# Kernel optimization log

Hardware: AMD Instinct MI355X
Metric: run time of the kernel (lower is better)

## Reference

```python
import jax, jax.numpy as jnp
import numpy as np

B, S, H, A = 64, 2048, 512, 512


def setup_inputs() -> dict:
    key = jax.random.key(0)
    k1, k2, k3, k4, k5 = jax.random.split(key, 5)
    nn_outs = jax.random.normal(k1, (B, S, H), dtype=jnp.float32)
    # lengths in [1, S] so every row has at least one valid step
    batch_lens = jax.random.randint(k2, (B,), 1, S + 1, dtype=jnp.int64)
    # learned params: context vector ~ U(-0.1, 0.1), Linear(H -> A)
    context = jax.random.uniform(k3, (A,), dtype=jnp.float32, minval=-0.1, maxval=0.1)
    proj_w = jax.random.uniform(k4, (A, H), dtype=jnp.float32, minval=-0.1, maxval=0.1)
    proj_b = jax.random.uniform(k5, (A,), dtype=jnp.float32, minval=-0.1, maxval=0.1)
    return {"nn_outs": nn_outs, "batch_lens": batch_lens,
            "context": context, "proj_w": proj_w, "proj_b": proj_b}


def reference(nn_outs, batch_lens, context, proj_w, proj_b):
    # proj = tanh(Linear(nn_outs)): (B, S, A)
    proj = jnp.tanh(jnp.einsum('bsh,ah->bsa', nn_outs, proj_w) + proj_b)
    # attention scores: (B, S)
    scores = jnp.einsum('bsa,a->bs', proj, context)
    # variable-length masked softmax (replaces the per-batch python loop)
    mask = jnp.arange(nn_outs.shape[1])[None, :] < batch_lens[:, None]  # (B, S)
    scores = jnp.where(mask, scores, -jnp.inf)
    atten = jax.nn.softmax(scores, axis=-1)
    atten = jnp.where(mask, atten, 0.0)  # padded positions exactly zero
    # weighted sum over steps: (B, H)
    return jnp.einsum('bs,bsh->bh', atten, nn_outs)
```

## Files before the change

kernel.cpp:

```cpp
#include <hip/hip_runtime.h>

#define BB 64
#define SS 2048
#define HH 512
#define MROWS (BB*SS)

typedef __attribute__((ext_vector_type(8))) short short8;
typedef __attribute__((ext_vector_type(4))) float f32x4;

__device__ inline unsigned short f2bf(float f){
  unsigned int u = __float_as_uint(f);
  u += 0x7FFFu + ((u >> 16) & 1u);
  return (unsigned short)(u >> 16);
}

__device__ inline int read_len(const void* lens, int i){
  const int* p = (const int*)lens;
  if (p[1] == 0) return (int)((const long long*)lens)[i];
  return p[i];
}

__device__ inline float fast_tanh(float x){
  x = fminf(fmaxf(x, -15.f), 15.f);
  float e = __expf(2.f * x);
  return (e - 1.f) / (e + 1.f);
}

__device__ inline void gload16(const void* gptr, void* lptr){
  __builtin_amdgcn_global_load_lds(
      (const __attribute__((address_space(1))) void*)gptr,
      (__attribute__((address_space(3))) void*)lptr, 16, 0, 0);
}

__device__ inline short8 cvt8p(float4 x0, float4 x1){
  short8 r;
  r[0] = (short)f2bf(x0.x); r[1] = (short)f2bf(x0.y);
  r[2] = (short)f2bf(x0.z); r[3] = (short)f2bf(x0.w);
  r[4] = (short)f2bf(x1.x); r[5] = (short)f2bf(x1.y);
  r[6] = (short)f2bf(x1.z); r[7] = (short)f2bf(x1.w);
  return r;
}

__global__ __launch_bounds__(256) void convw_kernel(
    const float* __restrict__ W, unsigned short* __restrict__ Wb)
{
  size_t base = (size_t)blockIdx.x * 64 * HH;
  int t = threadIdx.x;
  #pragma unroll
  for (int j = 0; j < 32; j++) {
    size_t idx = base + (size_t)j * 1024 + t * 4;
    float4 v = *(const float4*)(W + idx);
    unsigned int p0 = (unsigned int)f2bf(v.x) | ((unsigned int)f2bf(v.y) << 16);
    unsigned int p1 = (unsigned int)f2bf(v.z) | ((unsigned int)f2bf(v.w) << 16);
    *(uint2*)(Wb + idx) = make_uint2(p0, p1);
  }
}

__global__ __launch_bounds__(512, 2) void scores_fused(
    const float* __restrict__ X, const unsigned short* __restrict__ Wb,
    const void* __restrict__ lens, const float* __restrict__ ctx,
    const float* __restrict__ pb, float* __restrict__ P,
    float* __restrict__ pm, float* __restrict__ ps)
{
  int bid = blockIdx.x;
  int mtile = (bid & 7) * 128 + (bid >> 3);
  int s_start = (mtile * 128) & (SS - 1);
  int b = (mtile * 128) >> 11;
  int len = read_len(lens, b);
  if (s_start >= len) return;
  int cnt = min(128, len - s_start);

  __shared__ __align__(16) unsigned short As[128 * 64];
  __shared__ __align__(16) unsigned short Bs[2][512 * 64];

  int tid = threadIdx.x;
  int lane = tid & 63;
  int w = tid >> 6;
  int wm = w >> 2, wn = w & 3;
  int l15 = lane & 15, g = lane >> 4;

  f32x4 acc[4][8];
  #pragma unroll
  for (int i = 0; i < 4; i++)
    #pragma unroll
    for (int j = 0; j < 8; j++) acc[i][j] = (f32x4)0.f;

  int arow = tid >> 2;
  int alg0 = (tid & 3) * 2;
  const float* Ag = X + (size_t)(mtile * 128 + arow) * HH + alg0 * 8;
  int apg0 = (alg0)     ^ (arow & 7);
  int apg1 = (alg0 + 1) ^ (arow & 7);

  int brow = lane >> 3;
  int blg = (lane & 7) ^ brow;
  const unsigned short* Bg = Wb + (size_t)brow * HH + blg * 8;

  float4 ar[4];

#define A_ISSUE(KT) { const float* p_ = Ag + (KT); \
    ar[0] = *(const float4*)p_;       ar[1] = *(const float4*)(p_ + 4); \
    ar[2] = *(const float4*)(p_ + 8); ar[3] = *(const float4*)(p_ + 12); }

#define A_WRITE() { \
    *(short8*)&As[arow * 64 + apg0 * 8] = cvt8p(ar[0], ar[1]); \
    *(short8*)&As[arow * 64 + apg1 * 8] = cvt8p(ar[2], ar[3]); }

#define B_ISSUE(BUF, KT) { _Pragma("unroll") for (int i_ = 0; i_ < 8; i_++) { \
    int j_ = w * 8 + i_; \
    gload16(Bg + (size_t)(j_ * 8) * HH + (KT), &Bs[BUF][(j_ * 8) * 64]); } }

  A_ISSUE(0)
  B_ISSUE(0, 0)
  A_WRITE()
  __syncthreads();

  int cur = 0;
  for (int t = 0; t < 8; ++t) {
    if (t < 7) {
      A_ISSUE((t + 1) * 64)
      B_ISSUE(cur ^ 1, (t + 1) * 64)
    }
    #pragma unroll
    for (int kk = 0; kk < 64; kk += 32) {
      int ga = g + (kk >> 3);
      int pga = (ga ^ (l15 & 7)) * 8;
      short8 af[4];
      #pragma unroll
      for (int im = 0; im < 4; im++) {
        int r = wm * 64 + im * 16 + l15;
        af[im] = *(const short8*)&As[r * 64 + pga];
      }
      #pragma unroll
      for (int in = 0; in < 8; in++) {
        int r2 = wn * 128 + in * 16 + l15;
        short8 bfr = *(const short8*)&Bs[cur][r2 * 64 + pga];
        #pragma unroll
        for (int im = 0; im < 4; im++)
          acc[im][in] = __builtin_amdgcn_mfma_f32_16x16x32_bf16(
              af[im], bfr, acc[im][in], 0, 0, 0);
      }
    }
    __syncthreads();
    if (t < 7) A_WRITE()
    __syncthreads();
    cur ^= 1;
  }

  float pbv[8], ctxv[8];
  #pragma unroll
  for (int in = 0; in < 8; in++) {
    int a_g = wn * 128 + in * 16 + l15;
    pbv[in] = pb[a_g];
    ctxv[in] = ctx[a_g];
  }
  float* fb  = (float*)As;
  float* red  = fb;
  float* esh  = fb + 512;
  float* wrd  = fb + 640;
  float* wrd2 = fb + 642;
  f32x4* redp = (f32x4*)(fb + 1024);
  #pragma unroll
  for (int im = 0; im < 4; im++) {
    #pragma unroll
    for (int r = 0; r < 4; r++) {
      float rowsum = 0.f;
      #pragma unroll
      for (int in = 0; in < 8; in++)
        rowsum += fast_tanh(acc[im][in][r] + pbv[in]) * ctxv[in];
      #pragma unroll
      for (int m = 1; m < 16; m <<= 1)
        rowsum += __shfl_xor(rowsum, m, 64);
      if (l15 == 0)
        red[wn * 128 + wm * 64 + im * 16 + g * 4 + r] = rowsum;
    }
  }
  __syncthreads();

  float sc = 0.f;
  if (tid < 128)
    sc = red[tid] + red[128 + tid] + red[256 + tid] + red[384 + tid];
  float v = (tid < 128 && tid < cnt) ? sc : -1e30f;
  #pragma unroll
  for (int off = 1; off < 64; off <<= 1) v = fmaxf(v, __shfl_xor(v, off, 64));
  if (tid < 128 && (tid & 63) == 0) wrd[tid >> 6] = v;
  __syncthreads();
  float m_loc = fmaxf(wrd[0], wrd[1]);
  float e = 0.f;
  if (tid < 128) {
    e = (tid < cnt) ? __expf(sc - m_loc) : 0.f;
    esh[tid] = e;
  }
  float s1 = e;
  #pragma unroll
  for (int off = 1; off < 64; off <<= 1) s1 += __shfl_xor(s1, off, 64);
  if (tid < 128 && (tid & 63) == 0) wrd2[tid >> 6] = s1;
  __syncthreads();
  if (tid == 0) {
    pm[mtile] = m_loc;
    ps[mtile] = wrd2[0] + wrd2[1];
  }

  float* BsF = (float*)Bs;
  int rowoff = w * 2 + (lane >> 5);
  int coloff = (lane & 31) * 4;
  const float* Xb2 = X + (size_t)(mtile * 128) * HH;
  int sgrp = tid >> 5;
  int h4s  = tid & 31;
  for (int c = 0; c < 4; ++c) {
    #pragma unroll
    for (int i = 0; i < 8; i++) {
      gload16(Xb2 + (size_t)(i * 16 + rowoff) * HH + c * 128 + coloff,
              (char*)BsF + i * 8192 + w * 1024);
    }
    __syncthreads();
    f32x4 a4 = (f32x4)0.f;
    #pragma unroll
    for (int j = 0; j < 8; j++) {
      int s = sgrp + j * 16;
      float wv = esh[s];
      f32x4 xv = *(const f32x4*)&BsF[s * 128 + h4s * 4];
      a4[0] += wv * xv[0]; a4[1] += wv * xv[1];
      a4[2] += wv * xv[2]; a4[3] += wv * xv[3];
    }
    #pragma unroll
    for (int q = 0; q < 4; q++) a4[q] += __shfl_xor(a4[q], 32, 64);
    if (lane < 32) redp[w * 32 + lane] = a4;
    __syncthreads();
    if (tid < 32) {
      f32x4 s4 = redp[tid];
      #pragma unroll
      for (int q = 1; q < 8; q++) {
        f32x4 r4 = redp[q * 32 + tid];
        s4[0] += r4[0]; s4[1] += r4[1]; s4[2] += r4[2]; s4[3] += r4[3];
      }
      *(f32x4*)&P[(size_t)mtile * HH + c * 128 + tid * 4] = s4;
    }
  }
}

__global__ __launch_bounds__(512) void combine_kernel(
    const float* __restrict__ P, const float* __restrict__ pm,
    const float* __restrict__ ps, const void* __restrict__ lens,
    float* __restrict__ out)
{
  int b = blockIdx.x;
  int tid = threadIdx.x;
  int len = read_len(lens, b);
  int nblk = (len + 127) >> 7;
  float m = -1e30f;
  for (int k = 0; k < nblk; ++k) m = fmaxf(m, pm[b * 16 + k]);
  float S = 0.f, acc = 0.f;
  for (int k = 0; k < nblk; ++k) {
    float f = __expf(pm[b * 16 + k] - m);
    S += f * ps[b * 16 + k];
    acc += f * P[(size_t)(b * 16 + k) * HH + tid];
  }
  out[(size_t)b * HH + tid] = acc / S;
}

__global__ __launch_bounds__(256) void scores_fb(
    const float* __restrict__ X, const void* __restrict__ lens,
    const float* __restrict__ ctx, const float* __restrict__ W,
    const float* __restrict__ pb, float* __restrict__ sp)
{
  int bid = blockIdx.x;
  int wg = (bid & 7) * 512 + (bid >> 3);
  int ntile = wg & 3;
  int mtile = wg >> 2;
  int s_start = (mtile * 128) & (SS - 1);
  int b = (mtile * 128) >> 11;
  if (s_start >= read_len(lens, b)) return;

  __shared__ unsigned short As[128 * 72];
  __shared__ unsigned short Bs[128 * 72];

  int tid = threadIdx.x;
  int lane = tid & 63;
  int w = tid >> 6;
  int wm = w >> 1, wn = w & 1;
  int l15 = lane & 15, g = lane >> 4;

  f32x4 acc[4][4];
  #pragma unroll
  for (int i = 0; i < 4; i++)
    #pragma unroll
    for (int j = 0; j < 4; j++) acc[i][j] = (f32x4)0.f;

  int srow = tid >> 4;
  int scol = (tid & 15) * 4;
  const float* Xbase = X + (size_t)(mtile * 128) * HH;
  const float* Wbase = W + (size_t)(ntile * 128) * HH;

  for (int kt = 0; kt < HH; kt += 64) {
    #pragma unroll
    for (int i = 0; i < 8; i++) {
      int row = srow + i * 16;
      float4 va = *(const float4*)(Xbase + (size_t)row * HH + kt + scol);
      unsigned int p0 = (unsigned int)f2bf(va.x) | ((unsigned int)f2bf(va.y) << 16);
      unsigned int p1 = (unsigned int)f2bf(va.z) | ((unsigned int)f2bf(va.w) << 16);
      *(uint2*)&As[row * 72 + scol] = make_uint2(p0, p1);
      float4 vb = *(const float4*)(Wbase + (size_t)row * HH + kt + scol);
      unsigned int q0 = (unsigned int)f2bf(vb.x) | ((unsigned int)f2bf(vb.y) << 16);
      unsigned int q1 = (unsigned int)f2bf(vb.z) | ((unsigned int)f2bf(vb.w) << 16);
      *(uint2*)&Bs[row * 72 + scol] = make_uint2(q0, q1);
    }
    __syncthreads();
    #pragma unroll
    for (int kk = 0; kk < 64; kk += 32) {
      short8 af[4], bfr[4];
      int ko = kk + g * 8;
      #pragma unroll
      for (int im = 0; im < 4; im++)
        af[im] = *(const short8*)&As[(wm * 64 + im * 16 + l15) * 72 + ko];
      #pragma unroll
      for (int in = 0; in < 4; in++)
        bfr[in] = *(const short8*)&Bs[(wn * 64 + in * 16 + l15) * 72 + ko];
      #pragma unroll
      for (int im = 0; im < 4; im++)
        #pragma unroll
        for (int in = 0; in < 4; in++)
          acc[im][in] = __builtin_amdgcn_mfma_f32_16x16x32_bf16(
              af[im], bfr[in], acc[im][in], 0, 0, 0);
    }
    __syncthreads();
  }

  #pragma unroll
  for (int im = 0; im < 4; im++) {
    #pragma unroll
    for (int r = 0; r < 4; r++) {
      float rowsum = 0.f;
      #pragma unroll
      for (int in = 0; in < 4; in++) {
        int a_g = ntile * 128 + wn * 64 + in * 16 + l15;
        rowsum += fast_tanh(acc[im][in][r] + pb[a_g]) * ctx[a_g];
      }
      #pragma unroll
      for (int m = 1; m < 16; m <<= 1)
        rowsum += __shfl_xor(rowsum, m, 64);
      if (l15 == 0) {
        int rowg = mtile * 128 + wm * 64 + im * 16 + g * 4 + r;
        sp[(size_t)(ntile * 2 + wn) * MROWS + rowg] = rowsum;
      }
    }
  }
}

__global__ __launch_bounds__(256) void softmax8_kernel(
    const float* __restrict__ sp, const void* __restrict__ lens,
    float* __restrict__ wts)
{
  int b = blockIdx.x;
  int tid = threadIdx.x;
  int len = read_len(lens, b);
  float sc[8];
  #pragma unroll
  for (int i = 0; i < 8; i++) {
    int s = tid + i * 256;
    size_t row = (size_t)b * SS + s;
    float v = 0.f;
    #pragma unroll
    for (int p = 0; p < 8; p++) v += sp[(size_t)p * MROWS + row];
    sc[i] = v;
  }
  float m = -1e30f;
  #pragma unroll
  for (int i = 0; i < 8; i++)
    if (tid + i * 256 < len) m = fmaxf(m, sc[i]);
  #pragma unroll
  for (int off = 1; off < 64; off <<= 1) m = fmaxf(m, __shfl_xor(m, off, 64));
  __shared__ float redm[4];
  __shared__ float reds[4];
  int w = tid >> 6, lane = tid & 63;
  if (lane == 0) redm[w] = m;
  __syncthreads();
  m = fmaxf(fmaxf(redm[0], redm[1]), fmaxf(redm[2], redm[3]));
  float e[8]; float sum = 0.f;
  #pragma unroll
  for (int i = 0; i < 8; i++) {
    int s = tid + i * 256;
    e[i] = (s < len) ? __expf(sc[i] - m) : 0.f;
    sum += e[i];
  }
  #pragma unroll
  for (int off = 1; off < 64; off <<= 1) sum += __shfl_xor(sum, off, 64);
  if (lane == 0) reds[w] = sum;
  __syncthreads();
  sum = reds[0] + reds[1] + reds[2] + reds[3];
  float inv = 1.f / sum;
  #pragma unroll
  for (int i = 0; i < 8; i++) {
    int s = tid + i * 256;
    wts[(size_t)b * SS + s] = e[i] * inv;
  }
}

__global__ __launch_bounds__(256) void wsum_fb(
    const float* __restrict__ X, const float* __restrict__ wts,
    const void* __restrict__ lens, float* __restrict__ op)
{
  int sc = blockIdx.x;
  int b  = blockIdx.y;
  int tid = threadIdx.x;
  int s0 = sc * 128;
  int len = read_len(lens, b);
  int cnt = min(128, len - s0);
  float* o = op + ((size_t)sc * BB + b) * HH;
  if (cnt <= 0) {
    *(float2*)(o + tid * 2) = make_float2(0.f, 0.f);
    return;
  }
  __shared__ float wsh[128];
  __shared__ f32x4 red[128];
  if (tid < 128) wsh[tid] = wts[(size_t)b * SS + s0 + tid];
  __syncthreads();
  int h = (tid & 127) * 4;
  int sr = tid >> 7;
  f32x4 acc = (f32x4)0.f;
  for (int i = sr; i < cnt; i += 2) {
    float wv = wsh[i];
    const float* xr = X + ((size_t)b * SS + s0 + i) * HH + h;
    float4 xv = *(const float4*)xr;
    acc[0] += wv * xv.x;
    acc[1] += wv * xv.y;
    acc[2] += wv * xv.z;
    acc[3] += wv * xv.w;
  }
  if (sr == 1) red[tid & 127] = acc;
  __syncthreads();
  if (sr == 0) {
    f32x4 r2 = red[tid];
    acc[0] += r2[0]; acc[1] += r2[1]; acc[2] += r2[2]; acc[3] += r2[3];
    *(f32x4*)(o + h) = acc;
  }
}

__global__ __launch_bounds__(512) void reduce_kernel(
    const float* __restrict__ op, float* __restrict__ out)
{
  int b = blockIdx.x;
  int h = threadIdx.x;
  float v = 0.f;
  #pragma unroll
  for (int sc = 0; sc < 16; sc++) v += op[((size_t)sc * BB + b) * HH + h];
  out[(size_t)b * HH + h] = v;
}

extern "C" void kernel_launch(void* const* d_in, const int* in_sizes, int n_in,
                              void* d_out, int out_size, void* d_ws, size_t ws_size,
                              hipStream_t stream) {
  const float* X   = (const float*)d_in[0];
  const void*  lens = d_in[1];
  const float* ctx = (const float*)d_in[2];
  const float* W   = (const float*)d_in[3];
  const float* pb  = (const float*)d_in[4];
  float* out = (float*)d_out;

  char* ws = (char*)d_ws;
  const size_t WB_BYTES = (size_t)HH * HH * 2;
  const size_t P_BYTES  = 1024ull * HH * 4;
  const size_t PM_BYTES = 1024 * 4;
  const size_t NEED = WB_BYTES + P_BYTES + 2 * PM_BYTES;

  if (ws_size >= NEED) {
    unsigned short* Wb = (unsigned short*)ws;
    float* P  = (float*)(ws + WB_BYTES);
    float* pm = (float*)(ws + WB_BYTES + P_BYTES);
    float* ps = (float*)(ws + WB_BYTES + P_BYTES + PM_BYTES);

    convw_kernel<<<8, 256, 0, stream>>>(W, Wb);
    scores_fused<<<1024, 512, 0, stream>>>(X, Wb, lens, ctx, pb, P, pm, ps);
    combine_kernel<<<BB, 512, 0, stream>>>(P, pm, ps, lens, out);
  } else {
    const size_t SP_BYTES = 8ull * MROWS * 4;
    const size_t WT_BYTES = (size_t)BB * SS * 4;
    float* sp  = (float*)ws;
    float* wts = (float*)(ws + SP_BYTES);
    float* op  = (float*)(ws + SP_BYTES + WT_BYTES);

    scores_fb<<<4096, 256, 0, stream>>>(X, lens, ctx, W, pb, sp);
    softmax8_kernel<<<BB, 256, 0, stream>>>(sp, lens, wts);
    wsum_fb<<<dim3(16, BB), 256, 0, stream>>>(X, wts, lens, op);
    reduce_kernel<<<BB, 512, 0, stream>>>(op, out);
  }
}
```

Before: 129.9 us.

## Double-buffer A tile and split GEMM k-loop into four barrier-phased MFMA stages

```diff
diff --git a/kernel.cpp b/kernel.cpp
--- a/kernel.cpp
+++ b/kernel.cpp
@@ -70,7 +70,7 @@
   if (s_start >= len) return;
   int cnt = min(128, len - s_start);
 
-  __shared__ __align__(16) unsigned short As[128 * 64];
+  __shared__ __align__(16) unsigned short As[2][128 * 64];
   __shared__ __align__(16) unsigned short Bs[2][512 * 64];
 
   int tid = threadIdx.x;
@@ -101,48 +101,107 @@
     ar[0] = *(const float4*)p_;       ar[1] = *(const float4*)(p_ + 4); \
     ar[2] = *(const float4*)(p_ + 8); ar[3] = *(const float4*)(p_ + 12); }
 
-#define A_WRITE() { \
-    *(short8*)&As[arow * 64 + apg0 * 8] = cvt8p(ar[0], ar[1]); \
-    *(short8*)&As[arow * 64 + apg1 * 8] = cvt8p(ar[2], ar[3]); }
-
-#define B_ISSUE(BUF, KT) { _Pragma("unroll") for (int i_ = 0; i_ < 8; i_++) { \
-    int j_ = w * 8 + i_; \
+#define A_WRITE(BUF) { \
+    *(short8*)&As[BUF][arow * 64 + apg0 * 8] = cvt8p(ar[0], ar[1]); \
+    *(short8*)&As[BUF][arow * 64 + apg1 * 8] = cvt8p(ar[2], ar[3]); }
+
+#define B_ISSUE4(BUF, KT, H) { _Pragma("unroll") for (int i_ = 0; i_ < 4; i_++) { \
+    int j_ = w * 8 + (H) * 4 + i_; \
     gload16(Bg + (size_t)(j_ * 8) * HH + (KT), &Bs[BUF][(j_ * 8) * 64]); } }
 
   A_ISSUE(0)
-  B_ISSUE(0, 0)
-  A_WRITE()
-  __syncthreads();
+  B_ISSUE4(0, 0, 0)
+  B_ISSUE4(0, 0, 1)
+  A_WRITE(0)
+  asm volatile("s_waitcnt lgkmcnt(0)" ::: "memory");
+  __builtin_amdgcn_s_barrier();
+
+  int pga0 = (g ^ (l15 & 7)) * 8;
+  int pga1 = ((g + 4) ^ (l15 & 7)) * 8;
 
   int cur = 0;
   for (int t = 0; t < 8; ++t) {
-    if (t < 7) {
-      A_ISSUE((t + 1) * 64)
-      B_ISSUE(cur ^ 1, (t + 1) * 64)
-    }
-    #pragma unroll
-    for (int kk = 0; kk < 64; kk += 32) {
-      int ga = g + (kk >> 3);
-      int pga = (ga ^ (l15 & 7)) * 8;
-      short8 af[4];
-      #pragma unroll
-      for (int im = 0; im < 4; im++) {
-        int r = wm * 64 + im * 16 + l15;
-        af[im] = *(const short8*)&As[r * 64 + pga];
-      }
-      #pragma unroll
-      for (int in = 0; in < 8; in++) {
-        int r2 = wn * 128 + in * 16 + l15;
-        short8 bfr = *(const short8*)&Bs[cur][r2 * 64 + pga];
-        #pragma unroll
-        for (int im = 0; im < 4; im++)
-          acc[im][in] = __builtin_amdgcn_mfma_f32_16x16x32_bf16(
-              af[im], bfr, acc[im][in], 0, 0, 0);
-      }
-    }
-    __syncthreads();
-    if (t < 7) A_WRITE()
-    __syncthreads();
+    int nxt = cur ^ 1;
+    bool pre = (t < 7);
+    short8 af[4], bq[4];
+
+    #pragma unroll
+    for (int im = 0; im < 4; im++)
+      af[im] = *(const short8*)&As[cur][(wm * 64 + im * 16 + l15) * 64 + pga0];
+    #pragma unroll
+    for (int in = 0; in < 4; in++)
+      bq[in] = *(const short8*)&Bs[cur][(wn * 128 + in * 16 + l15) * 64 + pga0];
+    if (pre) { A_ISSUE((t + 1) * 64) B_ISSUE4(nxt, (t + 1) * 64, 0) }
+    __builtin_amdgcn_s_barrier();
+    asm volatile("s_waitcnt lgkmcnt(0)" ::: "memory");
+    __builtin_amdgcn_sched_barrier(0);
+    __builtin_amdgcn_s_setprio(1);
+    #pragma unroll
+    for (int in = 0; in < 4; in++)
+      #pragma unroll
+      for (int im = 0; im < 4; im++)
+        acc[im][in] = __builtin_amdgcn_mfma_f32_16x16x32_bf16(
+            af[im], bq[in], acc[im][in], 0, 0, 0);
+    __builtin_amdgcn_s_setprio(0);
+    __builtin_amdgcn_s_barrier();
+
+    #pragma unroll
+    for (int in = 0; in < 4; in++)
+      bq[in] = *(const short8*)&Bs[cur][(wn * 128 + (in + 4) * 16 + l15) * 64 + pga0];
+    if (pre) { B_ISSUE4(nxt, (t + 1) * 64, 1) }
+    __builtin_amdgcn_s_barrier();
+    asm volatile("s_waitcnt lgkmcnt(0)" ::: "memory");
+    __builtin_amdgcn_sched_barrier(0);
+    __builtin_amdgcn_s_setprio(1);
+    #pragma unroll
+    for (int in = 0; in < 4; in++)
+      #pragma unroll
+      for (int im = 0; im < 4; im++)
+        acc[im][in + 4] = __builtin_amdgcn_mfma_f32_16x16x32_bf16(
+            af[im], bq[in], acc[im][in + 4], 0, 0, 0);
+    __builtin_amdgcn_s_setprio(0);
+    __builtin_amdgcn_s_barrier();
+
+    #pragma unroll
+    for (int im = 0; im < 4; im++)
+      af[im] = *(const short8*)&As[cur][(wm * 64 + im * 16 + l15) * 64 + pga1];
+    #pragma unroll
+    for (int in = 0; in < 4; in++)
+      bq[in] = *(const short8*)&Bs[cur][(wn * 128 + in * 16 + l15) * 64 + pga1];
+    __builtin_amdgcn_s_barrier();
+    asm volatile("s_waitcnt lgkmcnt(0)" ::: "memory");
+    __builtin_amdgcn_sched_barrier(0);
+    __builtin_amdgcn_s_setprio(1);
+    #pragma unroll
+    for (int in = 0; in < 4; in++)
+      #pragma unroll
+      for (int im = 0; im < 4; im++)
+        acc[im][in] = __builtin_amdgcn_mfma_f32_16x16x32_bf16(
+            af[im], bq[in], acc[im][in], 0, 0, 0);
+    __builtin_amdgcn_s_setprio(0);
+    __builtin_amdgcn_s_barrier();
+
+    #pragma unroll
+    for (int in = 0; in < 4; in++)
+      bq[in] = *(const short8*)&Bs[cur][(wn * 128 + (in + 4) * 16 + l15) * 64 + pga1];
+    if (pre) {
+      asm volatile("s_waitcnt vmcnt(0)" ::: "memory");
+      A_WRITE(nxt)
+      asm volatile("s_waitcnt lgkmcnt(0)" ::: "memory");
+    }
+    __builtin_amdgcn_s_barrier();
+    asm volatile("s_waitcnt lgkmcnt(0)" ::: "memory");
+    __builtin_amdgcn_sched_barrier(0);
+    __builtin_amdgcn_s_setprio(1);
+    #pragma unroll
+    for (int in = 0; in < 4; in++)
+      #pragma unroll
+      for (int im = 0; im < 4; im++)
+        acc[im][in + 4] = __builtin_amdgcn_mfma_f32_16x16x32_bf16(
+            af[im], bq[in], acc[im][in + 4], 0, 0, 0);
+    __builtin_amdgcn_s_setprio(0);
+    __builtin_amdgcn_s_barrier();
+
     cur ^= 1;
   }
 
```

After: 131.8 us. No clear change (+1.4%).

## Keep full bf16 X tile in LDS and reuse it for weighted sum

Applied to the files above, without the earlier changes.

```diff
diff --git a/kernel.cpp b/kernel.cpp
--- a/kernel.cpp
+++ b/kernel.cpp
@@ -12,6 +12,9 @@
   unsigned int u = __float_as_uint(f);
   u += 0x7FFFu + ((u >> 16) & 1u);
   return (unsigned short)(u >> 16);
+}
+__device__ inline float bf2f(unsigned short u){
+  return __uint_as_float((unsigned int)u << 16);
 }
 
 __device__ inline int read_len(const void* lens, int i){
@@ -56,6 +59,8 @@
   }
 }
 
+#define AS_IDX(SL, ROW, PG) ((SL) * 4096 + (ROW) * 32 + (PG) * 8)
+
 __global__ __launch_bounds__(512, 2) void scores_fused(
     const float* __restrict__ X, const unsigned short* __restrict__ Wb,
     const void* __restrict__ lens, const float* __restrict__ ctx,
@@ -70,8 +75,8 @@
   if (s_start >= len) return;
   int cnt = min(128, len - s_start);
 
-  __shared__ __align__(16) unsigned short As[128 * 64];
-  __shared__ __align__(16) unsigned short Bs[2][512 * 64];
+  __shared__ __align__(16) unsigned short As[16 * 4096];
+  __shared__ __align__(16) unsigned short Bs[512 * 32];
 
   int tid = threadIdx.x;
   int lane = tid & 63;
@@ -79,71 +84,54 @@
   int wm = w >> 2, wn = w & 3;
   int l15 = lane & 15, g = lane >> 4;
 
+  {
+    int arow = tid >> 2;
+    int alg  = tid & 3;
+    int apg  = alg ^ (arow & 3);
+    const float* Ag = X + (size_t)(mtile * 128 + arow) * HH + alg * 8;
+    #pragma unroll
+    for (int s = 0; s < 16; s++) {
+      float4 x0 = *(const float4*)(Ag + s * 32);
+      float4 x1 = *(const float4*)(Ag + s * 32 + 4);
+      *(short8*)&As[AS_IDX(s, arow, apg)] = cvt8p(x0, x1);
+    }
+  }
+
   f32x4 acc[4][8];
   #pragma unroll
   for (int i = 0; i < 4; i++)
     #pragma unroll
     for (int j = 0; j < 8; j++) acc[i][j] = (f32x4)0.f;
 
-  int arow = tid >> 2;
-  int alg0 = (tid & 3) * 2;
-  const float* Ag = X + (size_t)(mtile * 128 + arow) * HH + alg0 * 8;
-  int apg0 = (alg0)     ^ (arow & 7);
-  int apg1 = (alg0 + 1) ^ (arow & 7);
-
-  int brow = lane >> 3;
-  int blg = (lane & 7) ^ brow;
-  const unsigned short* Bg = Wb + (size_t)brow * HH + blg * 8;
-
-  float4 ar[4];
-
-#define A_ISSUE(KT) { const float* p_ = Ag + (KT); \
-    ar[0] = *(const float4*)p_;       ar[1] = *(const float4*)(p_ + 4); \
-    ar[2] = *(const float4*)(p_ + 8); ar[3] = *(const float4*)(p_ + 12); }
-
-#define A_WRITE() { \
-    *(short8*)&As[arow * 64 + apg0 * 8] = cvt8p(ar[0], ar[1]); \
-    *(short8*)&As[arow * 64 + apg1 * 8] = cvt8p(ar[2], ar[3]); }
-
-#define B_ISSUE(BUF, KT) { _Pragma("unroll") for (int i_ = 0; i_ < 8; i_++) { \
-    int j_ = w * 8 + i_; \
-    gload16(Bg + (size_t)(j_ * 8) * HH + (KT), &Bs[BUF][(j_ * 8) * 64]); } }
-
-  A_ISSUE(0)
-  B_ISSUE(0, 0)
-  A_WRITE()
-  __syncthreads();
-
-  int cur = 0;
-  for (int t = 0; t < 8; ++t) {
-    if (t < 7) {
-      A_ISSUE((t + 1) * 64)
-      B_ISSUE(cur ^ 1, (t + 1) * 64)
-    }
-    #pragma unroll
-    for (int kk = 0; kk < 64; kk += 32) {
-      int ga = g + (kk >> 3);
-      int pga = (ga ^ (l15 & 7)) * 8;
-      short8 af[4];
-      #pragma unroll
-      for (int im = 0; im < 4; im++) {
-        int r = wm * 64 + im * 16 + l15;
-        af[im] = *(const short8*)&As[r * 64 + pga];
-      }
-      #pragma unroll
-      for (int in = 0; in < 8; in++) {
-        int r2 = wn * 128 + in * 16 + l15;
-        short8 bfr = *(const short8*)&Bs[cur][r2 * 64 + pga];
-        #pragma unroll
-        for (int im = 0; im < 4; im++)
-          acc[im][in] = __builtin_amdgcn_mfma_f32_16x16x32_bf16(
-              af[im], bfr, acc[im][in], 0, 0, 0);
-      }
+  int brow_i = lane >> 2;
+  int bpg    = lane & 3;
+  int cur_row_lo = w * 64;
+
+  for (int t = 0; t < 16; ++t) {
+    #pragma unroll
+    for (int i_ = 0; i_ < 4; i_++) {
+      int base = cur_row_lo + i_ * 16;
+      int row = base + brow_i;
+      int blg = bpg ^ (row & 3);
+      gload16(Wb + (size_t)row * HH + t * 32 + blg * 8, &Bs[base * 32]);
     }
     __syncthreads();
-    if (t < 7) A_WRITE()
+    short8 af[4];
+    #pragma unroll
+    for (int im = 0; im < 4; im++) {
+      int r = wm * 64 + im * 16 + l15;
+      af[im] = *(const short8*)&As[AS_IDX(t, r, g ^ (r & 3))];
+    }
+    #pragma unroll
+    for (int in = 0; in < 8; in++) {
+      int r2 = wn * 128 + in * 16 + l15;
+      short8 bq = *(const short8*)&Bs[r2 * 32 + ((g ^ (r2 & 3))) * 8];
+      #pragma unroll
+      for (int im = 0; im < 4; im++)
+        acc[im][in] = __builtin_amdgcn_mfma_f32_16x16x32_bf16(
+            af[im], bq, acc[im][in], 0, 0, 0);
+    }
     __syncthreads();
-    cur ^= 1;
   }
 
   float pbv[8], ctxv[8];
@@ -153,12 +141,12 @@
     pbv[in] = pb[a_g];
     ctxv[in] = ctx[a_g];
   }
-  float* fb  = (float*)As;
+  float* fb   = (float*)Bs;
   float* red  = fb;
   float* esh  = fb + 512;
   float* wrd  = fb + 640;
   float* wrd2 = fb + 642;
-  f32x4* redp = (f32x4*)(fb + 1024);
+  float* redq = fb + 1024;
   #pragma unroll
   for (int im = 0; im < 4; im++) {
     #pragma unroll
@@ -200,41 +188,38 @@
     ps[mtile] = wrd2[0] + wrd2[1];
   }
 
-  float* BsF = (float*)Bs;
-  int rowoff = w * 2 + (lane >> 5);
-  int coloff = (lane & 31) * 4;
-  const float* Xb2 = X + (size_t)(mtile * 128) * HH;
-  int sgrp = tid >> 5;
-  int h4s  = tid & 31;
-  for (int c = 0; c < 4; ++c) {
-    #pragma unroll
-    for (int i = 0; i < 8; i++) {
-      gload16(Xb2 + (size_t)(i * 16 + rowoff) * HH + c * 128 + coloff,
-              (char*)BsF + i * 8192 + w * 1024);
-    }
-    __syncthreads();
-    f32x4 a4 = (f32x4)0.f;
-    #pragma unroll
-    for (int j = 0; j < 8; j++) {
-      int s = sgrp + j * 16;
-      float wv = esh[s];
-      f32x4 xv = *(const f32x4*)&BsF[s * 128 + h4s * 4];
-      a4[0] += wv * xv[0]; a4[1] += wv * xv[1];
-      a4[2] += wv * xv[2]; a4[3] += wv * xv[3];
-    }
-    #pragma unroll
-    for (int q = 0; q < 4; q++) a4[q] += __shfl_xor(a4[q], 32, 64);
-    if (lane < 32) redp[w * 32 + lane] = a4;
-    __syncthreads();
-    if (tid < 32) {
-      f32x4 s4 = redp[tid];
-      #pragma unroll
-      for (int q = 1; q < 8; q++) {
-        f32x4 r4 = redp[q * 32 + tid];
-        s4[0] += r4[0]; s4[1] += r4[1]; s4[2] += r4[2]; s4[3] += r4[3];
-      }
-      *(f32x4*)&P[(size_t)mtile * HH + c * 128 + tid * 4] = s4;
-    }
+  int oct = tid & 63;
+  int sg  = tid >> 6;
+  int slice = oct >> 2;
+  int lg2 = oct & 3;
+  float a8[8];
+  #pragma unroll
+  for (int q = 0; q < 8; q++) a8[q] = 0.f;
+  #pragma unroll
+  for (int j = 0; j < 16; j++) {
+    int s = sg + j * 8;
+    float wv = esh[s];
+    short8 xv = *(const short8*)&As[AS_IDX(slice, s, lg2 ^ (s & 3))];
+    #pragma unroll
+    for (int q = 0; q < 8; q++)
+      a8[q] += wv * bf2f((unsigned short)xv[q]);
+  }
+  #pragma unroll
+  for (int q = 0; q < 8; q++) redq[(size_t)sg * 512 + oct * 8 + q] = a8[q];
+  __syncthreads();
+  if (sg == 0) {
+    #pragma unroll
+    for (int q = 0; q < 8; q++) {
+      float s4 = 0.f;
+      #pragma unroll
+      for (int k = 0; k < 8; k++) s4 += redq[(size_t)k * 512 + oct * 8 + q];
+      a8[q] = s4;
+    }
+    f32x4 o0, o1;
+    o0[0] = a8[0]; o0[1] = a8[1]; o0[2] = a8[2]; o0[3] = a8[3];
+    o1[0] = a8[4]; o1[1] = a8[5]; o1[2] = a8[6]; o1[3] = a8[7];
+    *(f32x4*)&P[(size_t)mtile * HH + oct * 8]     = o0;
+    *(f32x4*)&P[(size_t)mtile * HH + oct * 8 + 4] = o1;
   }
 }
 
```

Result: slower. 132.8 us (+2.2%).
